# Kernel tuning notes

Hardware: AMD Instinct MI355X
Metric: run time of the kernel (lower is better)

Reference implementation:

```python
import jax, jax.numpy as jnp
import numpy as np

N = 100_000
E = 1_600_000
F_IN = 128
HID = 128
OUT = 64


def setup_inputs() -> dict:
    key = jax.random.key(0)
    k = jax.random.split(key, 6)
    x = jax.random.normal(k[0], (N, F_IN), dtype=jnp.float32)
    edge_index = jax.random.randint(k[1], (2, E), 0, N, dtype=jnp.int64)
    edge_weight = jax.random.uniform(k[2], (E,), dtype=jnp.float32)
    W1 = jax.random.normal(k[3], (F_IN, HID), dtype=jnp.float32) * (1.0 / np.sqrt(F_IN))
    b1 = jnp.zeros((HID,), dtype=jnp.float32)
    W2 = jax.random.normal(k[4], (HID, OUT), dtype=jnp.float32) * (1.0 / np.sqrt(HID))
    b2 = jnp.zeros((OUT,), dtype=jnp.float32)
    return {"x": x, "edge_index": edge_index, "edge_weight": edge_weight,
            "W1": W1, "b1": b1, "W2": W2, "b2": b2}


def reference(x, edge_index, edge_weight, W1, b1, W2, b2):
    n = x.shape[0]
    src, dst = edge_index[0], edge_index[1]
    # gcn_norm: add self-loops with weight 1
    loop = jnp.arange(n, dtype=src.dtype)
    src_f = jnp.concatenate([src, loop])          # [E+N]
    dst_f = jnp.concatenate([dst, loop])          # [E+N]
    w_f = jnp.concatenate([edge_weight, jnp.ones((n,), dtype=edge_weight.dtype)])
    # degree over target nodes, symmetric normalization D^-1/2 A D^-1/2
    deg = jax.ops.segment_sum(w_f, dst_f, num_segments=n)   # [N]
    dinv = jnp.where(deg > 0, jax.lax.rsqrt(deg), 0.0)
    norm = dinv[src_f] * w_f * dinv[dst_f]        # [E+N]
    # GCNConv: linear transform then normalized sparse aggregation + bias
    h = x @ W1                                    # [N, HID]
    msg = h[src_f] * norm[:, None]                # [E+N, HID] gather
    agg = jax.ops.segment_sum(msg, dst_f, num_segments=n) + b1  # scatter-add
    # ReLU + Linear
    return jax.nn.relu(agg) @ W2 + b2             # [N, OUT]
```

## Files before the change

### kernel.cpp

```cpp
#include <hip/hip_runtime.h>

#define N_NODES 100000
#define N_EDGES 1600000
#define F_IN    128
#define HID     128
#define F_OUT   64

#define NBUCK   196
#define NCHB    256
#define CHUNK_E (N_EDGES / NCHB)
#define GHN     (NBUCK * NCHB)

#define XB_BLKS (N_NODES * 16 / 256)
#define WC_BLKS ((HID * F_IN + F_OUT * HID + 255) / 256)

typedef __attribute__((ext_vector_type(8))) short bf16x8;
typedef __attribute__((ext_vector_type(4))) float f32x4;


__device__ __forceinline__ unsigned int bf16rn(float f) {
    unsigned int u = __float_as_uint(f);
    return (u + 0x7fffu + ((u >> 16) & 1u)) >> 16;
}
__device__ __forceinline__ float bf16tof(unsigned short h) {
    return __uint_as_float(((unsigned int)h) << 16);
}


__global__ __launch_bounds__(256) void k_pre(
        const float* __restrict__ x, unsigned short* __restrict__ xh,
        const float* __restrict__ W1, const float* __restrict__ W2,
        unsigned short* __restrict__ w1t, unsigned short* __restrict__ w2t,
        const int* __restrict__ dst, int* __restrict__ ghist) {
    __shared__ int bins[NBUCK];
    const int blk = blockIdx.x;
    const int t = threadIdx.x;
    if (blk < XB_BLKS) {
        int i = blk * 256 + t;
        float4 a = ((const float4*)x)[2 * i];
        float4 b = ((const float4*)x)[2 * i + 1];
        uint4 r;
        r.x = bf16rn(a.x) | (bf16rn(a.y) << 16);
        r.y = bf16rn(a.z) | (bf16rn(a.w) << 16);
        r.z = bf16rn(b.x) | (bf16rn(b.y) << 16);
        r.w = bf16rn(b.z) | (bf16rn(b.w) << 16);
        ((uint4*)xh)[i] = r;
    } else if (blk < XB_BLKS + WC_BLKS) {
        int i = (blk - XB_BLKS) * 256 + t;
        if (i < HID * F_IN) {
            int n = i >> 7, k = i & 127;
            w1t[i] = (unsigned short)bf16rn(W1[k * HID + n]);
        }
        int j = i - HID * F_IN;
        if (j >= 0 && j < F_OUT * HID) {
            int n = j >> 7, k = j & 127;
            w2t[j] = (unsigned short)bf16rn(W2[k * F_OUT + n]);
        }
    } else {
        int cb = blk - XB_BLKS - WC_BLKS;
        for (int j = t; j < NBUCK; j += 256) bins[j] = 0;
        __syncthreads();
        const int base = cb * CHUNK_E;
        for (int i = t; i < CHUNK_E; i += 256)
            atomicAdd(&bins[dst[base + i] >> 9], 1);
        __syncthreads();
        for (int j = t; j < NBUCK; j += 256)
            ghist[j * NCHB + cb] = bins[j];
    }
}


__global__ void k_scan_part(const int* __restrict__ data, int* __restrict__ part, int n) {
    int i = blockIdx.x * 256 + threadIdx.x;
    int v = (i < n) ? data[i] : 0;
    #pragma unroll
    for (int off = 32; off > 0; off >>= 1) v += __shfl_down(v, off, 64);
    __shared__ int ws[4];
    if ((threadIdx.x & 63) == 0) ws[threadIdx.x >> 6] = v;
    __syncthreads();
    if (threadIdx.x == 0) part[blockIdx.x] = ws[0] + ws[1] + ws[2] + ws[3];
}

__global__ __launch_bounds__(512) void k_scan_top(int* __restrict__ part, int nparts) {
    __shared__ int s[512];
    int t = threadIdx.x;
    int v = (t < nparts) ? part[t] : 0;
    s[t] = v;
    __syncthreads();
    for (int off = 1; off < 512; off <<= 1) {
        int u = (t >= off) ? s[t - off] : 0;
        __syncthreads();
        s[t] += u;
        __syncthreads();
    }
    if (t < nparts) part[t] = s[t] - v;
}

__global__ void k_scan_down(int* __restrict__ data, const int* __restrict__ part, int n) {
    __shared__ int s[256];
    int t = threadIdx.x;
    int i = blockIdx.x * 256 + t;
    int v = (i < n) ? data[i] : 0;
    s[t] = v;
    __syncthreads();
    for (int off = 1; off < 256; off <<= 1) {
        int u = (t >= off) ? s[t - off] : 0;
        __syncthreads();
        s[t] += u;
        __syncthreads();
    }
    if (i < n) data[i] = part[blockIdx.x] + s[t] - v;
}


__global__ __launch_bounds__(256) void k_bscatter(const int* __restrict__ src,
                                                  const int* __restrict__ dst,
                                                  const float* __restrict__ w,
                                                  const int* __restrict__ ghist,
                                                  int2* __restrict__ spw) {
    __shared__ int cur[NBUCK];
    const int t = threadIdx.x;
    const int blk = blockIdx.x;
    for (int j = t; j < NBUCK; j += 256) cur[j] = ghist[j * NCHB + blk];
    __syncthreads();
    const int base = blk * CHUNK_E;
    for (int i = t; i < CHUNK_E; i += 256) {
        int e = base + i;
        int d = dst[e];
        int b = d >> 9;
        int pos = atomicAdd(&cur[b], 1);
        int2 p;
        p.x = src[e] | ((d & 511) << 17);
        p.y = __float_as_int(w[e]);
        spw[pos] = p;
    }
}


__global__ __launch_bounds__(512) void k_csr(const int2* __restrict__ spw,
                                             const int* __restrict__ ghist,
                                             int* __restrict__ row_ptr,
                                             float* __restrict__ dinv,
                                             int2* __restrict__ pairs) {
    __shared__ int   scnt[512];
    __shared__ float swsum[512];
    __shared__ int   sexcl[512];
    const int t = threadIdx.x;
    const int b = blockIdx.x;
    const int bstart = ghist[b * NCHB];
    const int bend   = (b == NBUCK - 1) ? N_EDGES : ghist[(b + 1) * NCHB];
    const int ne = bend - bstart;

    scnt[t] = 0; swsum[t] = 0.0f;
    __syncthreads();
    for (int i = t; i < ne; i += 512) {
        int2 pe = spw[bstart + i];
        int dl = pe.x >> 17;
        atomicAdd(&scnt[dl], 1);
        atomicAdd(&swsum[dl], __int_as_float(pe.y));
    }
    __syncthreads();

    sexcl[t] = scnt[t];
    __syncthreads();
    for (int off = 1; off < 512; off <<= 1) {
        int u = (t >= off) ? sexcl[t - off] : 0;
        __syncthreads();
        sexcl[t] += u;
        __syncthreads();
    }
    int excl = sexcl[t] - scnt[t];

    int node = b * 512 + t;
    if (node < N_NODES) {
        row_ptr[node] = bstart + excl;
        dinv[node] = rsqrtf(1.0f + swsum[t]);
    }
    if (b == NBUCK - 1 && t == 0) row_ptr[N_NODES] = N_EDGES;

    sexcl[t] = excl;
    __syncthreads();
    scnt[t] = 0;
    __syncthreads();

    for (int i = t; i < ne; i += 512) {
        int2 pe = spw[bstart + i];
        int dl = pe.x >> 17;
        int r = atomicAdd(&scnt[dl], 1);
        int2 q;
        q.x = pe.x & 0x1FFFF;
        q.y = pe.y;
        pairs[bstart + sexcl[dl] + r] = q;
    }
}


__global__ __launch_bounds__(256) void k_gather(const int2* __restrict__ pairs,
                                                const int* __restrict__ row_ptr,
                                                const float* __restrict__ dinv,
                                                const unsigned short* __restrict__ xh,
                                                unsigned short* __restrict__ axh) {
    int t = blockIdx.x * 256 + threadIdx.x;
    int n = t >> 5;
    int lane = t & 31;
    if (n >= N_NODES) return;

    const ushort4* xh4 = (const ushort4*)xh;
    float dn = dinv[n];
    ushort4 sv = xh4[n * 32 + lane];
    float4 acc;
    acc.x = dn * bf16tof(sv.x);
    acc.y = dn * bf16tof(sv.y);
    acc.z = dn * bf16tof(sv.z);
    acc.w = dn * bf16tof(sv.w);

    int beg = row_ptr[n];
    int end = row_ptr[n + 1];
    int e = beg;
    for (; e + 3 < end; e += 4) {
        int2 p0 = pairs[e];
        int2 p1 = pairs[e + 1];
        int2 p2 = pairs[e + 2];
        int2 p3 = pairs[e + 3];
        float nw0 = dinv[p0.x] * __int_as_float(p0.y);
        float nw1 = dinv[p1.x] * __int_as_float(p1.y);
        float nw2 = dinv[p2.x] * __int_as_float(p2.y);
        float nw3 = dinv[p3.x] * __int_as_float(p3.y);
        ushort4 v0 = xh4[p0.x * 32 + lane];
        ushort4 v1 = xh4[p1.x * 32 + lane];
        ushort4 v2 = xh4[p2.x * 32 + lane];
        ushort4 v3 = xh4[p3.x * 32 + lane];
        acc.x += nw0 * bf16tof(v0.x); acc.y += nw0 * bf16tof(v0.y);
        acc.z += nw0 * bf16tof(v0.z); acc.w += nw0 * bf16tof(v0.w);
        acc.x += nw1 * bf16tof(v1.x); acc.y += nw1 * bf16tof(v1.y);
        acc.z += nw1 * bf16tof(v1.z); acc.w += nw1 * bf16tof(v1.w);
        acc.x += nw2 * bf16tof(v2.x); acc.y += nw2 * bf16tof(v2.y);
        acc.z += nw2 * bf16tof(v2.z); acc.w += nw2 * bf16tof(v2.w);
        acc.x += nw3 * bf16tof(v3.x); acc.y += nw3 * bf16tof(v3.y);
        acc.z += nw3 * bf16tof(v3.z); acc.w += nw3 * bf16tof(v3.w);
    }
    for (; e < end; ++e) {
        int2 p = pairs[e];
        float nw = dinv[p.x] * __int_as_float(p.y);
        ushort4 v = xh4[p.x * 32 + lane];
        acc.x += nw * bf16tof(v.x); acc.y += nw * bf16tof(v.y);
        acc.z += nw * bf16tof(v.z); acc.w += nw * bf16tof(v.w);
    }
    acc.x *= dn; acc.y *= dn; acc.z *= dn; acc.w *= dn;
    uint2 r;
    r.x = bf16rn(acc.x) | (bf16rn(acc.y) << 16);
    r.y = bf16rn(acc.z) | (bf16rn(acc.w) << 16);
    ((uint2*)axh)[n * 32 + lane] = r;
}


__global__ __launch_bounds__(256) void k_mlp(
        const unsigned short* __restrict__ axh,
        const unsigned short* __restrict__ w1t,
        const float* __restrict__ b1,
        const unsigned short* __restrict__ w2t,
        const float* __restrict__ b2,
        float* __restrict__ out) {
    __shared__ unsigned short hbuf[4][16][128];

    const int wid  = threadIdx.x >> 6;
    const int lane = threadIdx.x & 63;
    const int r = lane & 15;
    const int g = lane >> 4;

    const int row0 = (blockIdx.x * 4 + wid) * 16;
    const bool valid = (row0 + 16 <= N_NODES);
    const int row0s = valid ? row0 : 0;

    bf16x8 a[4];
    const unsigned short* arow = axh + (size_t)(row0s + r) * HID + g * 8;
    #pragma unroll
    for (int kt = 0; kt < 4; ++kt)
        a[kt] = *(const bf16x8*)(arow + kt * 32);

    const int swr = (r & 7) << 3;

    #pragma unroll
    for (int nt = 0; nt < 8; ++nt) {
        f32x4 acc = {0.f, 0.f, 0.f, 0.f};
        const unsigned short* bcol = w1t + (nt * 16 + r) * HID + g * 8;
        #pragma unroll
        for (int kt = 0; kt < 4; ++kt) {
            bf16x8 b = *(const bf16x8*)(bcol + kt * 32);
            acc = __builtin_amdgcn_mfma_f32_16x16x32_bf16(a[kt], b, acc, 0, 0, 0);
        }
        float bias = b1[nt * 16 + r];
        #pragma unroll
        for (int q = 0; q < 4; ++q) {
            int row = g * 4 + q;
            float v = fmaxf(acc[q] + bias, 0.0f);
            hbuf[wid][row][(nt * 16 + r) ^ ((row & 7) << 3)] = (unsigned short)bf16rn(v);
        }
    }
    __syncthreads();

    bf16x8 a2[4];
    #pragma unroll
    for (int kt = 0; kt < 4; ++kt)
        a2[kt] = *(const bf16x8*)(&hbuf[wid][r][(kt * 32 + g * 8) ^ swr]);

    #pragma unroll
    for (int nt = 0; nt < 4; ++nt) {
        f32x4 acc = {0.f, 0.f, 0.f, 0.f};
        const unsigned short* bcol = w2t + (nt * 16 + r) * HID + g * 8;
        #pragma unroll
        for (int kt = 0; kt < 4; ++kt) {
            bf16x8 b = *(const bf16x8*)(bcol + kt * 32);
            acc = __builtin_amdgcn_mfma_f32_16x16x32_bf16(a2[kt], b, acc, 0, 0, 0);
        }
        if (valid) {
            float bias = b2[nt * 16 + r];
            #pragma unroll
            for (int q = 0; q < 4; ++q)
                out[(size_t)(row0 + g * 4 + q) * F_OUT + nt * 16 + r] = acc[q] + bias;
        }
    }
}


extern "C" void kernel_launch(void* const* d_in, const int* in_sizes, int n_in,
                              void* d_out, int out_size, void* d_ws, size_t ws_size,
                              hipStream_t stream) {
    const float* x  = (const float*)d_in[0];
    const int*   ei = (const int*)d_in[1];
    const float* ew = (const float*)d_in[2];
    const float* W1 = (const float*)d_in[3];
    const float* b1 = (const float*)d_in[4];
    const float* W2 = (const float*)d_in[5];
    const float* b2 = (const float*)d_in[6];
    float* out = (float*)d_out;

    const int* src = ei;
    const int* dst = ei + N_EDGES;

    char* base = (char*)d_ws;
    auto alloc16 = [&](size_t bytes) { char* p = base; base += (bytes + 15) & ~(size_t)15; return p; };

    float*          dinv    = (float*)         alloc16(N_NODES * 4);
    unsigned short* xh      = (unsigned short*)alloc16((size_t)N_NODES * F_IN * 2);
    int*            row_ptr = (int*)           alloc16((N_NODES + 1) * 4);
    int*            ghist   = (int*)           alloc16(GHN * 4);
    int*            part    = (int*)           alloc16(256 * 4);
    int2*           pairs   = (int2*)          alloc16((size_t)N_EDGES * 8);
    char*           big     =                  alloc16((size_t)N_NODES * HID * 2);
    unsigned short* w1t     = (unsigned short*)alloc16(HID * F_IN * 2);
    unsigned short* w2t     = (unsigned short*)alloc16(F_OUT * HID * 2);

    int2*           spw     = (int2*)big;
    unsigned short* axh     = (unsigned short*)big;

    const int GH_BLKS = (GHN + 255) / 256;

    k_pre<<<XB_BLKS + WC_BLKS + NCHB, 256, 0, stream>>>(x, xh, W1, W2, w1t, w2t, dst, ghist);
    k_scan_part<<<GH_BLKS, 256, 0, stream>>>(ghist, part, GHN);
    k_scan_top<<<1, 512, 0, stream>>>(part, GH_BLKS);
    k_scan_down<<<GH_BLKS, 256, 0, stream>>>(ghist, part, GHN);
    k_bscatter<<<NCHB, 256, 0, stream>>>(src, dst, ew, ghist, spw);
    k_csr<<<NBUCK, 512, 0, stream>>>(spw, ghist, row_ptr, dinv, pairs);
    k_gather<<<(N_NODES * 32 + 255) / 256, 256, 0, stream>>>(pairs, row_ptr, dinv, xh, axh);
    k_mlp<<<(N_NODES / 16 + 3) / 4, 256, 0, stream>>>(axh, w1t, b1, w2t, b2, out);
}
```

Before: 187.4 us.

## Prescale features by dinv, merge scan kernels, stage bucket edges in LDS

Moves the source-side D^-1/2 scaling into a new pass that converts x to bf16 after dinv is known, so the gather no longer does a random dinv[src] load per edge. The three-kernel hierarchical scan becomes one kernel in which each block recomputes its prefix by re-reading earlier histogram entries. k_csr copies a bucket's edges into LDS when they fit, so the two passes over them avoid a second global read. The trade-offs are rounding to bf16 after scaling, a redundant O(n^2)-style prefix read in the scan, and about 74KB of LDS per csr block.

```diff
diff --git a/kernel.cpp b/kernel.cpp
--- a/kernel.cpp
+++ b/kernel.cpp
@@ -10,9 +10,10 @@
 #define NCHB    256
 #define CHUNK_E (N_EDGES / NCHB)
 #define GHN     (NBUCK * NCHB)
-
-#define XB_BLKS (N_NODES * 16 / 256)
+#define SCAN_BLKS (GHN / 256)
+
 #define WC_BLKS ((HID * F_IN + F_OUT * HID + 255) / 256)
+#define CSR_LDS 9216
 
 typedef __attribute__((ext_vector_type(8))) short bf16x8;
 typedef __attribute__((ext_vector_type(4))) float f32x4;
@@ -27,26 +28,15 @@
 }
 
 
-__global__ __launch_bounds__(256) void k_pre(
-        const float* __restrict__ x, unsigned short* __restrict__ xh,
+__global__ __launch_bounds__(256) void k_pre0(
         const float* __restrict__ W1, const float* __restrict__ W2,
         unsigned short* __restrict__ w1t, unsigned short* __restrict__ w2t,
         const int* __restrict__ dst, int* __restrict__ ghist) {
     __shared__ int bins[NBUCK];
     const int blk = blockIdx.x;
     const int t = threadIdx.x;
-    if (blk < XB_BLKS) {
+    if (blk < WC_BLKS) {
         int i = blk * 256 + t;
-        float4 a = ((const float4*)x)[2 * i];
-        float4 b = ((const float4*)x)[2 * i + 1];
-        uint4 r;
-        r.x = bf16rn(a.x) | (bf16rn(a.y) << 16);
-        r.y = bf16rn(a.z) | (bf16rn(a.w) << 16);
-        r.z = bf16rn(b.x) | (bf16rn(b.y) << 16);
-        r.w = bf16rn(b.z) | (bf16rn(b.w) << 16);
-        ((uint4*)xh)[i] = r;
-    } else if (blk < XB_BLKS + WC_BLKS) {
-        int i = (blk - XB_BLKS) * 256 + t;
         if (i < HID * F_IN) {
             int n = i >> 7, k = i & 127;
             w1t[i] = (unsigned short)bf16rn(W1[k * HID + n]);
@@ -57,7 +47,7 @@
             w2t[j] = (unsigned short)bf16rn(W2[k * F_OUT + n]);
         }
     } else {
-        int cb = blk - XB_BLKS - WC_BLKS;
+        int cb = blk - WC_BLKS;
         for (int j = t; j < NBUCK; j += 256) bins[j] = 0;
         __syncthreads();
         const int base = cb * CHUNK_E;
@@ -70,58 +60,45 @@
 }
 
 
-__global__ void k_scan_part(const int* __restrict__ data, int* __restrict__ part, int n) {
-    int i = blockIdx.x * 256 + threadIdx.x;
-    int v = (i < n) ? data[i] : 0;
-    #pragma unroll
-    for (int off = 32; off > 0; off >>= 1) v += __shfl_down(v, off, 64);
-    __shared__ int ws[4];
-    if ((threadIdx.x & 63) == 0) ws[threadIdx.x >> 6] = v;
-    __syncthreads();
-    if (threadIdx.x == 0) part[blockIdx.x] = ws[0] + ws[1] + ws[2] + ws[3];
-}
-
-__global__ __launch_bounds__(512) void k_scan_top(int* __restrict__ part, int nparts) {
-    __shared__ int s[512];
-    int t = threadIdx.x;
-    int v = (t < nparts) ? part[t] : 0;
-    s[t] = v;
-    __syncthreads();
-    for (int off = 1; off < 512; off <<= 1) {
-        int u = (t >= off) ? s[t - off] : 0;
-        __syncthreads();
-        s[t] += u;
-        __syncthreads();
-    }
-    if (t < nparts) part[t] = s[t] - v;
-}
-
-__global__ void k_scan_down(int* __restrict__ data, const int* __restrict__ part, int n) {
-    __shared__ int s[256];
-    int t = threadIdx.x;
-    int i = blockIdx.x * 256 + t;
-    int v = (i < n) ? data[i] : 0;
-    s[t] = v;
+__global__ __launch_bounds__(256) void k_scan(const int* __restrict__ ghist,
+                                              int* __restrict__ ghs) {
+    __shared__ int red[256];
+    const int t = threadIdx.x;
+    const int b = blockIdx.x;
+
+    int s = 0;
+    for (int i = t; i < b * 256; i += 256) s += ghist[i];
+    red[t] = s;
+    __syncthreads();
+    for (int off = 128; off > 0; off >>= 1) {
+        if (t < off) red[t] += red[t + off];
+        __syncthreads();
+    }
+    const int base = red[0];
+    __syncthreads();
+
+    int v = ghist[b * 256 + t];
+    red[t] = v;
     __syncthreads();
     for (int off = 1; off < 256; off <<= 1) {
-        int u = (t >= off) ? s[t - off] : 0;
-        __syncthreads();
-        s[t] += u;
-        __syncthreads();
-    }
-    if (i < n) data[i] = part[blockIdx.x] + s[t] - v;
+        int u = (t >= off) ? red[t - off] : 0;
+        __syncthreads();
+        red[t] += u;
+        __syncthreads();
+    }
+    ghs[b * 256 + t] = base + red[t] - v;
 }
 
 
 __global__ __launch_bounds__(256) void k_bscatter(const int* __restrict__ src,
                                                   const int* __restrict__ dst,
                                                   const float* __restrict__ w,
-                                                  const int* __restrict__ ghist,
+                                                  const int* __restrict__ ghs,
                                                   int2* __restrict__ spw) {
     __shared__ int cur[NBUCK];
     const int t = threadIdx.x;
     const int blk = blockIdx.x;
-    for (int j = t; j < NBUCK; j += 256) cur[j] = ghist[j * NCHB + blk];
+    for (int j = t; j < NBUCK; j += 256) cur[j] = ghs[j * NCHB + blk];
     __syncthreads();
     const int base = blk * CHUNK_E;
     for (int i = t; i < CHUNK_E; i += 256) {
@@ -138,23 +115,28 @@
 
 
 __global__ __launch_bounds__(512) void k_csr(const int2* __restrict__ spw,
-                                             const int* __restrict__ ghist,
+                                             const int* __restrict__ ghs,
                                              int* __restrict__ row_ptr,
                                              float* __restrict__ dinv,
                                              int2* __restrict__ pairs) {
     __shared__ int   scnt[512];
     __shared__ float swsum[512];
     __shared__ int   sexcl[512];
+    __shared__ int2  sspw[CSR_LDS];
     const int t = threadIdx.x;
     const int b = blockIdx.x;
-    const int bstart = ghist[b * NCHB];
-    const int bend   = (b == NBUCK - 1) ? N_EDGES : ghist[(b + 1) * NCHB];
+    const int bstart = ghs[b * NCHB];
+    const int bend   = (b == NBUCK - 1) ? N_EDGES : ghs[(b + 1) * NCHB];
     const int ne = bend - bstart;
+    const bool inlds = (ne <= CSR_LDS);
 
     scnt[t] = 0; swsum[t] = 0.0f;
-    __syncthreads();
+    if (inlds)
+        for (int i = t; i < ne; i += 512) sspw[i] = spw[bstart + i];
+    __syncthreads();
+
     for (int i = t; i < ne; i += 512) {
-        int2 pe = spw[bstart + i];
+        int2 pe = inlds ? sspw[i] : spw[bstart + i];
         int dl = pe.x >> 17;
         atomicAdd(&scnt[dl], 1);
         atomicAdd(&swsum[dl], __int_as_float(pe.y));
@@ -184,7 +166,7 @@
     __syncthreads();
 
     for (int i = t; i < ne; i += 512) {
-        int2 pe = spw[bstart + i];
+        int2 pe = inlds ? sspw[i] : spw[bstart + i];
         int dl = pe.x >> 17;
         int r = atomicAdd(&scnt[dl], 1);
         int2 q;
@@ -195,24 +177,42 @@
 }
 
 
+__global__ __launch_bounds__(256) void k_xhs(const float* __restrict__ x,
+                                             const float* __restrict__ dinv,
+                                             unsigned short* __restrict__ xhs) {
+    int i = blockIdx.x * 256 + threadIdx.x;
+    if (i < N_NODES * 16) {
+        float dn = dinv[i >> 4];
+        float4 a = ((const float4*)x)[2 * i];
+        float4 b = ((const float4*)x)[2 * i + 1];
+        uint4 r;
+        r.x = bf16rn(dn * a.x) | (bf16rn(dn * a.y) << 16);
+        r.y = bf16rn(dn * a.z) | (bf16rn(dn * a.w) << 16);
+        r.z = bf16rn(dn * b.x) | (bf16rn(dn * b.y) << 16);
+        r.w = bf16rn(dn * b.z) | (bf16rn(dn * b.w) << 16);
+        ((uint4*)xhs)[i] = r;
+    }
+}
+
+
 __global__ __launch_bounds__(256) void k_gather(const int2* __restrict__ pairs,
                                                 const int* __restrict__ row_ptr,
                                                 const float* __restrict__ dinv,
-                                                const unsigned short* __restrict__ xh,
+                                                const unsigned short* __restrict__ xhs,
                                                 unsigned short* __restrict__ axh) {
     int t = blockIdx.x * 256 + threadIdx.x;
     int n = t >> 5;
     int lane = t & 31;
     if (n >= N_NODES) return;
 
-    const ushort4* xh4 = (const ushort4*)xh;
+    const ushort4* xs4 = (const ushort4*)xhs;
     float dn = dinv[n];
-    ushort4 sv = xh4[n * 32 + lane];
+    ushort4 sv = xs4[n * 32 + lane];
     float4 acc;
-    acc.x = dn * bf16tof(sv.x);
-    acc.y = dn * bf16tof(sv.y);
-    acc.z = dn * bf16tof(sv.z);
-    acc.w = dn * bf16tof(sv.w);
+    acc.x = bf16tof(sv.x);
+    acc.y = bf16tof(sv.y);
+    acc.z = bf16tof(sv.z);
+    acc.w = bf16tof(sv.w);
 
     int beg = row_ptr[n];
     int end = row_ptr[n + 1];
@@ -222,29 +222,29 @@
         int2 p1 = pairs[e + 1];
         int2 p2 = pairs[e + 2];
         int2 p3 = pairs[e + 3];
-        float nw0 = dinv[p0.x] * __int_as_float(p0.y);
-        float nw1 = dinv[p1.x] * __int_as_float(p1.y);
-        float nw2 = dinv[p2.x] * __int_as_float(p2.y);
-        float nw3 = dinv[p3.x] * __int_as_float(p3.y);
-        ushort4 v0 = xh4[p0.x * 32 + lane];
-        ushort4 v1 = xh4[p1.x * 32 + lane];
-        ushort4 v2 = xh4[p2.x * 32 + lane];
-        ushort4 v3 = xh4[p3.x * 32 + lane];
-        acc.x += nw0 * bf16tof(v0.x); acc.y += nw0 * bf16tof(v0.y);
-        acc.z += nw0 * bf16tof(v0.z); acc.w += nw0 * bf16tof(v0.w);
-        acc.x += nw1 * bf16tof(v1.x); acc.y += nw1 * bf16tof(v1.y);
-        acc.z += nw1 * bf16tof(v1.z); acc.w += nw1 * bf16tof(v1.w);
-        acc.x += nw2 * bf16tof(v2.x); acc.y += nw2 * bf16tof(v2.y);
-        acc.z += nw2 * bf16tof(v2.z); acc.w += nw2 * bf16tof(v2.w);
-        acc.x += nw3 * bf16tof(v3.x); acc.y += nw3 * bf16tof(v3.y);
-        acc.z += nw3 * bf16tof(v3.z); acc.w += nw3 * bf16tof(v3.w);
+        float w0 = __int_as_float(p0.y);
+        float w1 = __int_as_float(p1.y);
+        float w2 = __int_as_float(p2.y);
+        float w3 = __int_as_float(p3.y);
+        ushort4 v0 = xs4[p0.x * 32 + lane];
+        ushort4 v1 = xs4[p1.x * 32 + lane];
+        ushort4 v2 = xs4[p2.x * 32 + lane];
+        ushort4 v3 = xs4[p3.x * 32 + lane];
+        acc.x += w0 * bf16tof(v0.x); acc.y += w0 * bf16tof(v0.y);
+        acc.z += w0 * bf16tof(v0.z); acc.w += w0 * bf16tof(v0.w);
+        acc.x += w1 * bf16tof(v1.x); acc.y += w1 * bf16tof(v1.y);
+        acc.z += w1 * bf16tof(v1.z); acc.w += w1 * bf16tof(v1.w);
+        acc.x += w2 * bf16tof(v2.x); acc.y += w2 * bf16tof(v2.y);
+        acc.z += w2 * bf16tof(v2.z); acc.w += w2 * bf16tof(v2.w);
+        acc.x += w3 * bf16tof(v3.x); acc.y += w3 * bf16tof(v3.y);
+        acc.z += w3 * bf16tof(v3.z); acc.w += w3 * bf16tof(v3.w);
     }
     for (; e < end; ++e) {
         int2 p = pairs[e];
-        float nw = dinv[p.x] * __int_as_float(p.y);
-        ushort4 v = xh4[p.x * 32 + lane];
-        acc.x += nw * bf16tof(v.x); acc.y += nw * bf16tof(v.y);
-        acc.z += nw * bf16tof(v.z); acc.w += nw * bf16tof(v.w);
+        float w = __int_as_float(p.y);
+        ushort4 v = xs4[p.x * 32 + lane];
+        acc.x += w * bf16tof(v.x); acc.y += w * bf16tof(v.y);
+        acc.z += w * bf16tof(v.z); acc.w += w * bf16tof(v.w);
     }
     acc.x *= dn; acc.y *= dn; acc.z *= dn; acc.w *= dn;
     uint2 r;
@@ -342,10 +342,10 @@
     auto alloc16 = [&](size_t bytes) { char* p = base; base += (bytes + 15) & ~(size_t)15; return p; };
 
     float*          dinv    = (float*)         alloc16(N_NODES * 4);
-    unsigned short* xh      = (unsigned short*)alloc16((size_t)N_NODES * F_IN * 2);
+    unsigned short* xhs     = (unsigned short*)alloc16((size_t)N_NODES * F_IN * 2);
     int*            row_ptr = (int*)           alloc16((N_NODES + 1) * 4);
     int*            ghist   = (int*)           alloc16(GHN * 4);
-    int*            part    = (int*)           alloc16(256 * 4);
+    int*            ghs     = (int*)           alloc16(GHN * 4);
     int2*           pairs   = (int2*)          alloc16((size_t)N_EDGES * 8);
     char*           big     =                  alloc16((size_t)N_NODES * HID * 2);
     unsigned short* w1t     = (unsigned short*)alloc16(HID * F_IN * 2);
@@ -354,14 +354,11 @@
     int2*           spw     = (int2*)big;
     unsigned short* axh     = (unsigned short*)big;
 
-    const int GH_BLKS = (GHN + 255) / 256;
-
-    k_pre<<<XB_BLKS + WC_BLKS + NCHB, 256, 0, stream>>>(x, xh, W1, W2, w1t, w2t, dst, ghist);
-    k_scan_part<<<GH_BLKS, 256, 0, stream>>>(ghist, part, GHN);
-    k_scan_top<<<1, 512, 0, stream>>>(part, GH_BLKS);
-    k_scan_down<<<GH_BLKS, 256, 0, stream>>>(ghist, part, GHN);
-    k_bscatter<<<NCHB, 256, 0, stream>>>(src, dst, ew, ghist, spw);
-    k_csr<<<NBUCK, 512, 0, stream>>>(spw, ghist, row_ptr, dinv, pairs);
-    k_gather<<<(N_NODES * 32 + 255) / 256, 256, 0, stream>>>(pairs, row_ptr, dinv, xh, axh);
+    k_pre0<<<WC_BLKS + NCHB, 256, 0, stream>>>(W1, W2, w1t, w2t, dst, ghist);
+    k_scan<<<SCAN_BLKS, 256, 0, stream>>>(ghist, ghs);
+    k_bscatter<<<NCHB, 256, 0, stream>>>(src, dst, ew, ghs, spw);
+    k_csr<<<NBUCK, 512, 0, stream>>>(spw, ghs, row_ptr, dinv, pairs);
+    k_xhs<<<(N_NODES * 16 + 255) / 256, 256, 0, stream>>>(x, dinv, xhs);
+    k_gather<<<(N_NODES * 32 + 255) / 256, 256, 0, stream>>>(pairs, row_ptr, dinv, xhs, axh);
     k_mlp<<<(N_NODES / 16 + 3) / 4, 256, 0, stream>>>(axh, w1t, b1, w2t, b2, out);
 }
```

After: 209.9 us. +12.0%, slower.

## Widen gather loads to 16 bytes and tile MLP over 64 rows per wave

Applied to the files above, without the earlier changes.

The gather kernel now gives each node 16 lanes, each loading 8 bf16 features as one 16-byte vector, instead of 32 lanes loading 4 each. This halves the threads per node and uses wider memory transactions. The MLP kernel now has each wave handle four 16-row tiles, loading each W1/W2 fragment once and reusing it across the four tiles. The per-wave LDS staging buffer grows fourfold to 64KB per block, which may lower occupancy, and the block-wide barrier is dropped because each wave only reads its own slice.

```diff
diff --git a/kernel.cpp b/kernel.cpp
--- a/kernel.cpp
+++ b/kernel.cpp
@@ -15,6 +15,7 @@
 #define WC_BLKS ((HID * F_IN + F_OUT * HID + 255) / 256)
 
 typedef __attribute__((ext_vector_type(8))) short bf16x8;
+typedef __attribute__((ext_vector_type(8))) unsigned short u16x8;
 typedef __attribute__((ext_vector_type(4))) float f32x4;
 
 
@@ -201,18 +202,16 @@
                                                 const unsigned short* __restrict__ xh,
                                                 unsigned short* __restrict__ axh) {
     int t = blockIdx.x * 256 + threadIdx.x;
-    int n = t >> 5;
-    int lane = t & 31;
+    int n = t >> 4;
+    int lane = t & 15;
     if (n >= N_NODES) return;
 
-    const ushort4* xh4 = (const ushort4*)xh;
+    const u16x8* xh8 = (const u16x8*)xh;
     float dn = dinv[n];
-    ushort4 sv = xh4[n * 32 + lane];
-    float4 acc;
-    acc.x = dn * bf16tof(sv.x);
-    acc.y = dn * bf16tof(sv.y);
-    acc.z = dn * bf16tof(sv.z);
-    acc.w = dn * bf16tof(sv.w);
+    u16x8 sv = xh8[n * 16 + lane];
+    float acc[8];
+    #pragma unroll
+    for (int j = 0; j < 8; ++j) acc[j] = dn * bf16tof(sv[j]);
 
     int beg = row_ptr[n];
     int end = row_ptr[n + 1];
@@ -226,31 +225,32 @@
         float nw1 = dinv[p1.x] * __int_as_float(p1.y);
         float nw2 = dinv[p2.x] * __int_as_float(p2.y);
         float nw3 = dinv[p3.x] * __int_as_float(p3.y);
-        ushort4 v0 = xh4[p0.x * 32 + lane];
-        ushort4 v1 = xh4[p1.x * 32 + lane];
-        ushort4 v2 = xh4[p2.x * 32 + lane];
-        ushort4 v3 = xh4[p3.x * 32 + lane];
-        acc.x += nw0 * bf16tof(v0.x); acc.y += nw0 * bf16tof(v0.y);
-        acc.z += nw0 * bf16tof(v0.z); acc.w += nw0 * bf16tof(v0.w);
-        acc.x += nw1 * bf16tof(v1.x); acc.y += nw1 * bf16tof(v1.y);
-        acc.z += nw1 * bf16tof(v1.z); acc.w += nw1 * bf16tof(v1.w);
-        acc.x += nw2 * bf16tof(v2.x); acc.y += nw2 * bf16tof(v2.y);
-        acc.z += nw2 * bf16tof(v2.z); acc.w += nw2 * bf16tof(v2.w);
-        acc.x += nw3 * bf16tof(v3.x); acc.y += nw3 * bf16tof(v3.y);
-        acc.z += nw3 * bf16tof(v3.z); acc.w += nw3 * bf16tof(v3.w);
+        u16x8 v0 = xh8[p0.x * 16 + lane];
+        u16x8 v1 = xh8[p1.x * 16 + lane];
+        u16x8 v2 = xh8[p2.x * 16 + lane];
+        u16x8 v3 = xh8[p3.x * 16 + lane];
+        #pragma unroll
+        for (int j = 0; j < 8; ++j) acc[j] += nw0 * bf16tof(v0[j]);
+        #pragma unroll
+        for (int j = 0; j < 8; ++j) acc[j] += nw1 * bf16tof(v1[j]);
+        #pragma unroll
+        for (int j = 0; j < 8; ++j) acc[j] += nw2 * bf16tof(v2[j]);
+        #pragma unroll
+        for (int j = 0; j < 8; ++j) acc[j] += nw3 * bf16tof(v3[j]);
     }
     for (; e < end; ++e) {
         int2 p = pairs[e];
         float nw = dinv[p.x] * __int_as_float(p.y);
-        ushort4 v = xh4[p.x * 32 + lane];
-        acc.x += nw * bf16tof(v.x); acc.y += nw * bf16tof(v.y);
-        acc.z += nw * bf16tof(v.z); acc.w += nw * bf16tof(v.w);
-    }
-    acc.x *= dn; acc.y *= dn; acc.z *= dn; acc.w *= dn;
-    uint2 r;
-    r.x = bf16rn(acc.x) | (bf16rn(acc.y) << 16);
-    r.y = bf16rn(acc.z) | (bf16rn(acc.w) << 16);
-    ((uint2*)axh)[n * 32 + lane] = r;
+        u16x8 v = xh8[p.x * 16 + lane];
+        #pragma unroll
+        for (int j = 0; j < 8; ++j) acc[j] += nw * bf16tof(v[j]);
+    }
+    uint4 r;
+    r.x = bf16rn(dn * acc[0]) | (bf16rn(dn * acc[1]) << 16);
+    r.y = bf16rn(dn * acc[2]) | (bf16rn(dn * acc[3]) << 16);
+    r.z = bf16rn(dn * acc[4]) | (bf16rn(dn * acc[5]) << 16);
+    r.w = bf16rn(dn * acc[6]) | (bf16rn(dn * acc[7]) << 16);
+    ((uint4*)axh)[n * 16 + lane] = r;
 }
 
 
@@ -261,63 +261,84 @@
         const unsigned short* __restrict__ w2t,
         const float* __restrict__ b2,
         float* __restrict__ out) {
-    __shared__ unsigned short hbuf[4][16][128];
+    __shared__ unsigned short hbuf[4][64][128];
 
     const int wid  = threadIdx.x >> 6;
     const int lane = threadIdx.x & 63;
     const int r = lane & 15;
     const int g = lane >> 4;
-
-    const int row0 = (blockIdx.x * 4 + wid) * 16;
-    const bool valid = (row0 + 16 <= N_NODES);
-    const int row0s = valid ? row0 : 0;
-
-    bf16x8 a[4];
-    const unsigned short* arow = axh + (size_t)(row0s + r) * HID + g * 8;
-    #pragma unroll
-    for (int kt = 0; kt < 4; ++kt)
-        a[kt] = *(const bf16x8*)(arow + kt * 32);
-
     const int swr = (r & 7) << 3;
 
+    const int row0 = (blockIdx.x * 4 + wid) * 64;
+
+    bool vld[4];
+    int rbase[4];
+    #pragma unroll
+    for (int rt = 0; rt < 4; ++rt) {
+        vld[rt] = (row0 + rt * 16 + 16 <= N_NODES);
+        rbase[rt] = vld[rt] ? (row0 + rt * 16) : 0;
+    }
+
+    bf16x8 a1[4][4];
+    #pragma unroll
+    for (int rt = 0; rt < 4; ++rt) {
+        const unsigned short* arow = axh + (size_t)(rbase[rt] + r) * HID + g * 8;
+        #pragma unroll
+        for (int kt = 0; kt < 4; ++kt)
+            a1[rt][kt] = *(const bf16x8*)(arow + kt * 32);
+    }
+
     #pragma unroll
     for (int nt = 0; nt < 8; ++nt) {
-        f32x4 acc = {0.f, 0.f, 0.f, 0.f};
+        bf16x8 b[4];
         const unsigned short* bcol = w1t + (nt * 16 + r) * HID + g * 8;
         #pragma unroll
-        for (int kt = 0; kt < 4; ++kt) {
-            bf16x8 b = *(const bf16x8*)(bcol + kt * 32);
-            acc = __builtin_amdgcn_mfma_f32_16x16x32_bf16(a[kt], b, acc, 0, 0, 0);
+        for (int kt = 0; kt < 4; ++kt)
+            b[kt] = *(const bf16x8*)(bcol + kt * 32);
+        float bias = b1[nt * 16 + r];
+        #pragma unroll
+        for (int rt = 0; rt < 4; ++rt) {
+            f32x4 acc = {0.f, 0.f, 0.f, 0.f};
+            #pragma unroll
+            for (int kt = 0; kt < 4; ++kt)
+                acc = __builtin_amdgcn_mfma_f32_16x16x32_bf16(a1[rt][kt], b[kt], acc, 0, 0, 0);
+            #pragma unroll
+            for (int q = 0; q < 4; ++q) {
+                int row16 = g * 4 + q;
+                float v = fmaxf(acc[q] + bias, 0.0f);
+                hbuf[wid][rt * 16 + row16][(nt * 16 + r) ^ ((row16 & 7) << 3)] =
+                    (unsigned short)bf16rn(v);
+            }
         }
-        float bias = b1[nt * 16 + r];
-        #pragma unroll
-        for (int q = 0; q < 4; ++q) {
-            int row = g * 4 + q;
-            float v = fmaxf(acc[q] + bias, 0.0f);
-            hbuf[wid][row][(nt * 16 + r) ^ ((row & 7) << 3)] = (unsigned short)bf16rn(v);
-        }
-    }
-    __syncthreads();
-
-    bf16x8 a2[4];
-    #pragma unroll
-    for (int kt = 0; kt < 4; ++kt)
-        a2[kt] = *(const bf16x8*)(&hbuf[wid][r][(kt * 32 + g * 8) ^ swr]);
+    }
+
+    bf16x8 a2[4][4];
+    #pragma unroll
+    for (int rt = 0; rt < 4; ++rt)
+        #pragma unroll
+        for (int kt = 0; kt < 4; ++kt)
+            a2[rt][kt] = *(const bf16x8*)(&hbuf[wid][rt * 16 + r][(kt * 32 + g * 8) ^ swr]);
 
     #pragma unroll
     for (int nt = 0; nt < 4; ++nt) {
-        f32x4 acc = {0.f, 0.f, 0.f, 0.f};
+        bf16x8 b[4];
         const unsigned short* bcol = w2t + (nt * 16 + r) * HID + g * 8;
         #pragma unroll
-        for (int kt = 0; kt < 4; ++kt) {
-            bf16x8 b = *(const bf16x8*)(bcol + kt * 32);
-            acc = __builtin_amdgcn_mfma_f32_16x16x32_bf16(a2[kt], b, acc, 0, 0, 0);
-        }
-        if (valid) {
-            float bias = b2[nt * 16 + r];
+        for (int kt = 0; kt < 4; ++kt)
+            b[kt] = *(const bf16x8*)(bcol + kt * 32);
+        float bias = b2[nt * 16 + r];
+        #pragma unroll
+        for (int rt = 0; rt < 4; ++rt) {
+            f32x4 acc = {0.f, 0.f, 0.f, 0.f};
             #pragma unroll
-            for (int q = 0; q < 4; ++q)
-                out[(size_t)(row0 + g * 4 + q) * F_OUT + nt * 16 + r] = acc[q] + bias;
+            for (int kt = 0; kt < 4; ++kt)
+                acc = __builtin_amdgcn_mfma_f32_16x16x32_bf16(a2[rt][kt], b[kt], acc, 0, 0, 0);
+            if (vld[rt]) {
+                #pragma unroll
+                for (int q = 0; q < 4; ++q)
+                    out[(size_t)(row0 + rt * 16 + g * 4 + q) * F_OUT + nt * 16 + r] =
+                        acc[q] + bias;
+            }
         }
     }
 }
@@ -362,6 +383,6 @@
     k_scan_down<<<GH_BLKS, 256, 0, stream>>>(ghist, part, GHN);
     k_bscatter<<<NCHB, 256, 0, stream>>>(src, dst, ew, ghist, spw);
     k_csr<<<NBUCK, 512, 0, stream>>>(spw, ghist, row_ptr, dinv, pairs);
-    k_gather<<<(N_NODES * 32 + 255) / 256, 256, 0, stream>>>(pairs, row_ptr, dinv, xh, axh);
-    k_mlp<<<(N_NODES / 16 + 3) / 4, 256, 0, stream>>>(axh, w1t, b1, w2t, b2, out);
-}
+    k_gather<<<(N_NODES * 16 + 255) / 256, 256, 0, stream>>>(pairs, row_ptr, dinv, xh, axh);
+    k_mlp<<<(N_NODES + 255) / 256, 256, 0, stream>>>(axh, w1t, b1, w2t, b2, out);
+}
```

Result: faster. 157.5 us (-16.0%).
